# Kernel optimization log

Measured on AMD Instinct MI355X. Metric: run time of the kernel, lower is better.

## Reference

```python
import jax, jax.numpy as jnp
import numpy as np

N_NODES = 100000
N_EDGES = 1600000
D_IN = 128
D_OUT = 128
EPS = 1e-12  # F.normalize default eps


def setup_inputs() -> dict:
    key = jax.random.key(0)
    k1, k2, k3, k4, k5 = jax.random.split(key, 5)
    x = jax.random.normal(k1, (N_NODES, D_IN), dtype=jnp.float32)
    edge_index = jax.random.randint(k2, (2, N_EDGES), 0, N_NODES, dtype=jnp.int64)
    # PyG SAGEConv params: lin_l (neighbor path, with bias), lin_r (root path, no bias)
    s = 1.0 / np.sqrt(D_IN)
    W_l = jax.random.uniform(k3, (D_IN, D_OUT), jnp.float32, -s, s)
    b_l = jax.random.uniform(k4, (D_OUT,), jnp.float32, -s, s)
    W_r = jax.random.uniform(k5, (D_IN, D_OUT), jnp.float32, -s, s)
    return {"x": x, "edge_index": edge_index, "W_l": W_l, "b_l": b_l, "W_r": W_r}


def reference(x, edge_index, W_l, b_l, W_r):
    n = x.shape[0]
    src = edge_index[0]  # message source nodes (x_j)
    dst = edge_index[1]  # aggregation targets (i)
    # gather + mean scatter-reduce
    msg = x[src]                                            # [E, D_IN]
    summed = jax.ops.segment_sum(msg, dst, num_segments=n)  # [N, D_IN]
    cnt = jax.ops.segment_sum(jnp.ones((msg.shape[0],), x.dtype), dst, num_segments=n)
    mean = summed / jnp.maximum(cnt, 1.0)[:, None]
    # lin_l(mean) + lin_r(x), then row-wise L2 normalize
    out = mean @ W_l + b_l + x @ W_r                        # [N, D_OUT]
    norm = jnp.sqrt(jnp.sum(out * out, axis=-1, keepdims=True))
    return out / jnp.maximum(norm, EPS)
```

## Files before the change

### kernel.cpp

```cpp
#include <hip/hip_runtime.h>
#include <hip/hip_bf16.h>

#define N_NODES 100000
#define N_EDGES 1600000
#define D 128
#define TILES (N_NODES / 16)
#define WPB 8
#define NB2 782
#define NPB2 128
#define CAP 4096
#define EPB 8192
#define PBLK 196
#define CVTB 6250
#define PREPB 128

typedef __attribute__((ext_vector_type(4))) float f32x4;
typedef __attribute__((ext_vector_type(8))) short short8;
typedef __attribute__((ext_vector_type(4))) unsigned int u32x4;
typedef __attribute__((ext_vector_type(2))) unsigned int u32x2;

static __device__ __forceinline__ unsigned short f2bf(float f) {
  unsigned u = __float_as_uint(f);
  u += 0x7fffu + ((u >> 16) & 1u);
  return (unsigned short)(u >> 16);
}

static __device__ __forceinline__ void acc4(u32x2 u, float& a0, float& a1,
                                            float& a2, float& a3) {
  a0 += __uint_as_float(u[0] << 16);
  a1 += __uint_as_float(u[0] & 0xffff0000u);
  a2 += __uint_as_float(u[1] << 16);
  a3 += __uint_as_float(u[1] & 0xffff0000u);
}

__global__ __launch_bounds__(256) void fuseA_k(
    const float* __restrict__ x, unsigned* __restrict__ xh,
    const int* __restrict__ ei, int* __restrict__ btail,
    unsigned* __restrict__ part, const float* __restrict__ Wl,
    const float* __restrict__ Wr, unsigned short* __restrict__ wt_g) {
  __shared__ int bh[NB2], lbase[NB2], lcur[NB2];
  int t = threadIdx.x;
  if (blockIdx.x < CVTB) {
    size_t i = (size_t)blockIdx.x * 256 + t;
    const f32x4* p = (const f32x4*)(x + i * 8);
    f32x4 v0 = p[0], v1 = p[1];
    u32x4 o;
    o[0] = ((unsigned)f2bf(v0[1]) << 16) | f2bf(v0[0]);
    o[1] = ((unsigned)f2bf(v0[3]) << 16) | f2bf(v0[2]);
    o[2] = ((unsigned)f2bf(v1[1]) << 16) | f2bf(v1[0]);
    o[3] = ((unsigned)f2bf(v1[3]) << 16) | f2bf(v1[2]);
    *(u32x4*)(xh + i * 4) = o;
    return;
  }
  if (blockIdx.x >= CVTB + PBLK) {
    int i = (blockIdx.x - CVTB - PBLK) * 256 + t;
    int k = i >> 7, c = i & 127;
    float w = (k < 128) ? Wl[k * 128 + c] : Wr[(k - 128) * 128 + c];
    int phys = (k >> 3) ^ (c & 7);
    wt_g[c * 256 + (phys << 3) + (k & 7)] = f2bf(w);
    return;
  }
  for (int i = t; i < NB2; i += 256) { bh[i] = 0; lcur[i] = 0; }
  __syncthreads();
  int base = (blockIdx.x - CVTB) * EPB;
  int end = min(base + EPB, N_EDGES);
  for (int i = base + t; i < end; i += 256)
    atomicAdd(&bh[ei[N_EDGES + i] >> 7], 1);
  __syncthreads();
  for (int i = t; i < NB2; i += 256)
    if (bh[i]) lbase[i] = atomicAdd(&btail[i], bh[i]);
  __syncthreads();
  for (int i = base + t; i < end; i += 256) {
    int dst = ei[N_EDGES + i];
    int src = ei[i];
    int b = dst >> 7;
    int pos = lbase[b] + atomicAdd(&lcur[b], 1);
    if (pos < CAP)
      part[(size_t)b * CAP + pos] =
          ((unsigned)(dst & (NPB2 - 1)) << 17) | (unsigned)src;
  }
}

__global__ __launch_bounds__(512) void p4c_k(unsigned* __restrict__ part,
                                             const int* __restrict__ btail,
                                             int2* __restrict__ pd) {
  __shared__ unsigned s_codes[CAP];
  __shared__ int s_deg[NPB2], s_scan[NPB2], s_off[NPB2];
  int t = threadIdx.x, b = blockIdx.x;
  int ne = min(btail[b], CAP);
  unsigned* pp = part + (size_t)b * CAP;
  for (int i = t; i < ne; i += 512) s_codes[i] = pp[i];
  if (t < NPB2) s_deg[t] = 0;
  __syncthreads();
  for (int i = t; i < ne; i += 512) atomicAdd(&s_deg[s_codes[i] >> 17], 1);
  __syncthreads();
  if (t < NPB2) s_scan[t] = s_deg[t];
  __syncthreads();
  for (int o = 1; o < NPB2; o <<= 1) {
    int u = (t >= o && t < NPB2) ? s_scan[t - o] : 0;
    __syncthreads();
    if (t < NPB2) s_scan[t] += u;
    __syncthreads();
  }
  if (t < NPB2) {
    int deg = s_deg[t];
    int ex = s_scan[t] - deg;
    s_off[t] = ex;
    int node = b * NPB2 + t;
    if (node < N_NODES) {
      int2 v;
      v.x = b * CAP + ex;
      v.y = deg;
      pd[node] = v;
    }
  }
  __syncthreads();
  for (int i = t; i < ne; i += 512) {
    unsigned c = s_codes[i];
    int pos = atomicAdd(&s_off[c >> 17], 1);
    pp[pos] = c & 0x1FFFFu;
  }
}

__global__ __launch_bounds__(256) void gather2_k(const unsigned* __restrict__ xh,
                                                 const unsigned* __restrict__ csr,
                                                 const int2* __restrict__ pd,
                                                 unsigned* __restrict__ mh) {
  int wid = (blockIdx.x * 256 + threadIdx.x) >> 6;
  int lane = threadIdx.x & 63;
  int half = lane >> 5, lh = lane & 31;
  int node = wid * 2 + half;
  if (node >= N_NODES) return;
  int2 v = pd[node];
  int base = v.x;
  int deg = v.y;
  float a0 = 0.f, a1 = 0.f, a2 = 0.f, a3 = 0.f;
  float b0 = 0.f, b1 = 0.f, b2 = 0.f, b3 = 0.f;
  for (int c = 0; c < deg; c += 32) {
    int rem = deg - c;
    int n = min(32, rem);
    int eidx = (lh < rem) ? (int)csr[base + c + lh] : 0;
    int j = 0;
    for (; j + 7 < n; j += 8) {
      int s0 = __shfl(eidx, j, 32);
      int s1 = __shfl(eidx, j + 1, 32);
      int s2 = __shfl(eidx, j + 2, 32);
      int s3 = __shfl(eidx, j + 3, 32);
      int s4 = __shfl(eidx, j + 4, 32);
      int s5 = __shfl(eidx, j + 5, 32);
      int s6 = __shfl(eidx, j + 6, 32);
      int s7 = __shfl(eidx, j + 7, 32);
      u32x2 u0 = *(const u32x2*)(xh + (size_t)s0 * 64 + lh * 2);
      u32x2 u1 = *(const u32x2*)(xh + (size_t)s1 * 64 + lh * 2);
      u32x2 u2 = *(const u32x2*)(xh + (size_t)s2 * 64 + lh * 2);
      u32x2 u3 = *(const u32x2*)(xh + (size_t)s3 * 64 + lh * 2);
      u32x2 u4 = *(const u32x2*)(xh + (size_t)s4 * 64 + lh * 2);
      u32x2 u5 = *(const u32x2*)(xh + (size_t)s5 * 64 + lh * 2);
      u32x2 u6 = *(const u32x2*)(xh + (size_t)s6 * 64 + lh * 2);
      u32x2 u7 = *(const u32x2*)(xh + (size_t)s7 * 64 + lh * 2);
      acc4(u0, a0, a1, a2, a3);
      acc4(u1, b0, b1, b2, b3);
      acc4(u2, a0, a1, a2, a3);
      acc4(u3, b0, b1, b2, b3);
      acc4(u4, a0, a1, a2, a3);
      acc4(u5, b0, b1, b2, b3);
      acc4(u6, a0, a1, a2, a3);
      acc4(u7, b0, b1, b2, b3);
    }
    for (; j + 3 < n; j += 4) {
      int s0 = __shfl(eidx, j, 32);
      int s1 = __shfl(eidx, j + 1, 32);
      int s2 = __shfl(eidx, j + 2, 32);
      int s3 = __shfl(eidx, j + 3, 32);
      u32x2 u0 = *(const u32x2*)(xh + (size_t)s0 * 64 + lh * 2);
      u32x2 u1 = *(const u32x2*)(xh + (size_t)s1 * 64 + lh * 2);
      u32x2 u2 = *(const u32x2*)(xh + (size_t)s2 * 64 + lh * 2);
      u32x2 u3 = *(const u32x2*)(xh + (size_t)s3 * 64 + lh * 2);
      acc4(u0, a0, a1, a2, a3);
      acc4(u1, b0, b1, b2, b3);
      acc4(u2, a0, a1, a2, a3);
      acc4(u3, b0, b1, b2, b3);
    }
    for (; j < n; j++) {
      int s0 = __shfl(eidx, j, 32);
      u32x2 u0 = *(const u32x2*)(xh + (size_t)s0 * 64 + lh * 2);
      acc4(u0, a0, a1, a2, a3);
    }
  }
  float inv = 1.0f / fmaxf((float)deg, 1.0f);
  a0 = (a0 + b0) * inv;
  a1 = (a1 + b1) * inv;
  a2 = (a2 + b2) * inv;
  a3 = (a3 + b3) * inv;
  u32x2 o;
  o[0] = ((unsigned)f2bf(a1) << 16) | f2bf(a0);
  o[1] = ((unsigned)f2bf(a3) << 16) | f2bf(a2);
  *(u32x2*)(mh + (size_t)node * 64 + lh * 2) = o;
}

__global__ __launch_bounds__(512) void fused_k(
    const unsigned* __restrict__ xh, const unsigned* __restrict__ mh,
    const unsigned* __restrict__ wt_g, const float* __restrict__ bl,
    float* __restrict__ out) {
  __shared__ unsigned Wt[16384];

  int tid = threadIdx.x;
  {
    const u32x4* src = (const u32x4*)wt_g;
    u32x4* dst = (u32x4*)Wt;
    #pragma unroll
    for (int it = 0; it < 8; it++) dst[it * 512 + tid] = src[it * 512 + tid];
  }
  __syncthreads();

  int tile = blockIdx.x * WPB + (tid >> 6);
  if (tile >= TILES) return;
  int lane = tid & 63;
  int c0 = lane & 15;
  int g = lane >> 4;
  int row0 = tile * 16;
  const unsigned short* Wt16 = (const unsigned short*)Wt;

  f32x4 acc[8];
  #pragma unroll
  for (int ct = 0; ct < 8; ct++)
    for (int j = 0; j < 4; j++) acc[ct][j] = 0.0f;

  #pragma unroll
  for (int kf = 0; kf < 8; kf++) {
    int koff = (kf & 3) * 32 + g * 8;
    const unsigned short* a_src = (const unsigned short*)((kf < 4) ? mh : xh);
    short8 af = *(const short8*)(a_src + (size_t)(row0 + c0) * D + koff);
    #pragma unroll
    for (int ct = 0; ct < 8; ct++) {
      int c = ct * 16 + c0;
      short8 bf = *(const short8*)&Wt16[c * 256 + ((((kf << 2) + g) ^ (c & 7)) << 3)];
      acc[ct] = __builtin_amdgcn_mfma_f32_16x16x32_bf16(af, bf, acc[ct], 0, 0, 0);
    }
  }

  float ss[4] = {0.f, 0.f, 0.f, 0.f};
  #pragma unroll
  for (int ct = 0; ct < 8; ct++) {
    float bias = bl[ct * 16 + c0];
    #pragma unroll
    for (int j = 0; j < 4; j++) {
      float v = acc[ct][j] + bias;
      acc[ct][j] = v;
      ss[j] += v * v;
    }
  }
  #pragma unroll
  for (int j = 0; j < 4; j++) {
    float s = ss[j];
    s += __shfl_xor(s, 1);
    s += __shfl_xor(s, 2);
    s += __shfl_xor(s, 4);
    s += __shfl_xor(s, 8);
    ss[j] = 1.0f / fmaxf(sqrtf(s), 1e-12f);
  }
  #pragma unroll
  for (int ct = 0; ct < 8; ct++) {
    #pragma unroll
    for (int j = 0; j < 4; j++) {
      out[(size_t)(row0 + g * 4 + j) * D + ct * 16 + c0] = acc[ct][j] * ss[j];
    }
  }
}

extern "C" void kernel_launch(void* const* d_in, const int* in_sizes, int n_in,
                              void* d_out, int out_size, void* d_ws, size_t ws_size,
                              hipStream_t stream) {
  const float* x  = (const float*)d_in[0];
  const int*   ei = (const int*)d_in[1];
  const float* Wl = (const float*)d_in[2];
  const float* bl = (const float*)d_in[3];
  const float* Wr = (const float*)d_in[4];
  float* out = (float*)d_out;

  int* w = (int*)d_ws;
  int* btail = w;
  int2* pd = (int2*)(w + 800);
  unsigned* part = (unsigned*)(w + 200800);
  unsigned short* wt_g = (unsigned short*)(w + 3403872);
  const size_t XH_OFF = 3420256ULL * 4;
  const size_t MH_OFF = XH_OFF + (size_t)N_NODES * D * 2;
  unsigned* xh = (unsigned*)((char*)d_ws + XH_OFF);
  unsigned* mh = (unsigned*)((char*)d_ws + MH_OFF);

  hipMemsetAsync(btail, 0, 800 * sizeof(int), stream);
  fuseA_k<<<CVTB + PBLK + PREPB, 256, 0, stream>>>(x, xh, ei, btail, part,
                                                   Wl, Wr, wt_g);
  p4c_k<<<NB2, 512, 0, stream>>>(part, btail, pd);
  gather2_k<<<12500, 256, 0, stream>>>(xh, part, pd, mh);
  fused_k<<<(TILES + WPB - 1) / WPB, 512, 0, stream>>>(xh, mh, (const unsigned*)wt_g, bl, out);
}
```

Baseline: 152.6 us.

## Replace atomic bucket reservation with per-block histogram and scan partitioning

Splits the fused convert and partition kernel into a conversion kernel plus a three-pass histogram, column scan and scatter. The global atomic reservation on per-bucket tails and its memset go away, and each block's offsets become deterministic, so edges land in source order within each bucket. In exchange it adds three extra kernel launches, reads the edge indices twice, and the partitioning no longer overlaps with the x conversion blocks.

```diff
diff --git a/kernel.cpp b/kernel.cpp
--- a/kernel.cpp
+++ b/kernel.cpp
@@ -33,12 +33,11 @@
   a3 += __uint_as_float(u[1] & 0xffff0000u);
 }
 
-__global__ __launch_bounds__(256) void fuseA_k(
-    const float* __restrict__ x, unsigned* __restrict__ xh,
-    const int* __restrict__ ei, int* __restrict__ btail,
-    unsigned* __restrict__ part, const float* __restrict__ Wl,
-    const float* __restrict__ Wr, unsigned short* __restrict__ wt_g) {
-  __shared__ int bh[NB2], lbase[NB2], lcur[NB2];
+__global__ __launch_bounds__(256) void cvtw_k(const float* __restrict__ x,
+                                              unsigned* __restrict__ xh,
+                                              const float* __restrict__ Wl,
+                                              const float* __restrict__ Wr,
+                                              unsigned short* __restrict__ wt_g) {
   int t = threadIdx.x;
   if (blockIdx.x < CVTB) {
     size_t i = (size_t)blockIdx.x * 256 + t;
@@ -52,42 +51,74 @@
     *(u32x4*)(xh + i * 4) = o;
     return;
   }
-  if (blockIdx.x >= CVTB + PBLK) {
-    int i = (blockIdx.x - CVTB - PBLK) * 256 + t;
-    int k = i >> 7, c = i & 127;
-    float w = (k < 128) ? Wl[k * 128 + c] : Wr[(k - 128) * 128 + c];
-    int phys = (k >> 3) ^ (c & 7);
-    wt_g[c * 256 + (phys << 3) + (k & 7)] = f2bf(w);
-    return;
-  }
-  for (int i = t; i < NB2; i += 256) { bh[i] = 0; lcur[i] = 0; }
-  __syncthreads();
-  int base = (blockIdx.x - CVTB) * EPB;
+  int i = (blockIdx.x - CVTB) * 256 + t;
+  int k = i >> 7, c = i & 127;
+  float w = (k < 128) ? Wl[k * 128 + c] : Wr[(k - 128) * 128 + c];
+  int phys = (k >> 3) ^ (c & 7);
+  wt_g[c * 256 + (phys << 3) + (k & 7)] = f2bf(w);
+}
+
+__global__ __launch_bounds__(256) void p1h_k(const int* __restrict__ ei,
+                                             int* __restrict__ hist) {
+  __shared__ int bh[NB2];
+  int t = threadIdx.x;
+  for (int i = t; i < NB2; i += 256) bh[i] = 0;
+  __syncthreads();
+  int base = blockIdx.x * EPB;
   int end = min(base + EPB, N_EDGES);
   for (int i = base + t; i < end; i += 256)
     atomicAdd(&bh[ei[N_EDGES + i] >> 7], 1);
   __syncthreads();
-  for (int i = t; i < NB2; i += 256)
-    if (bh[i]) lbase[i] = atomicAdd(&btail[i], bh[i]);
-  __syncthreads();
+  for (int i = t; i < NB2; i += 256) hist[blockIdx.x * NB2 + i] = bh[i];
+}
+
+__global__ __launch_bounds__(256) void scanb_k(int* __restrict__ hist,
+                                               int* __restrict__ bcnt) {
+  __shared__ int s[256];
+  int b = blockIdx.x, t = threadIdx.x;
+  int v = (t < PBLK) ? hist[t * NB2 + b] : 0;
+  s[t] = v;
+  __syncthreads();
+  for (int o = 1; o < 256; o <<= 1) {
+    int u = (t >= o) ? s[t - o] : 0;
+    __syncthreads();
+    s[t] += u;
+    __syncthreads();
+  }
+  if (t < PBLK) hist[t * NB2 + b] = s[t] - v;
+  if (t == 0) bcnt[b] = min(s[255], CAP);
+}
+
+__global__ __launch_bounds__(256) void p3c_k(const int* __restrict__ ei,
+                                             const int* __restrict__ hist,
+                                             unsigned* __restrict__ part) {
+  __shared__ int lbase[NB2], lcur[NB2];
+  int t = threadIdx.x, blk = blockIdx.x;
+  for (int i = t; i < NB2; i += 256) {
+    lbase[i] = hist[blk * NB2 + i];
+    lcur[i] = 0;
+  }
+  __syncthreads();
+  int base = blk * EPB;
+  int end = min(base + EPB, N_EDGES);
   for (int i = base + t; i < end; i += 256) {
     int dst = ei[N_EDGES + i];
     int src = ei[i];
     int b = dst >> 7;
-    int pos = lbase[b] + atomicAdd(&lcur[b], 1);
-    if (pos < CAP)
-      part[(size_t)b * CAP + pos] =
+    int rel = lbase[b] + atomicAdd(&lcur[b], 1);
+    if (rel < CAP)
+      part[(size_t)b * CAP + rel] =
           ((unsigned)(dst & (NPB2 - 1)) << 17) | (unsigned)src;
   }
 }
 
 __global__ __launch_bounds__(512) void p4c_k(unsigned* __restrict__ part,
-                                             const int* __restrict__ btail,
+                                             const int* __restrict__ bcnt,
                                              int2* __restrict__ pd) {
   __shared__ unsigned s_codes[CAP];
   __shared__ int s_deg[NPB2], s_scan[NPB2], s_off[NPB2];
   int t = threadIdx.x, b = blockIdx.x;
-  int ne = min(btail[b], CAP);
+  int ne = min(bcnt[b], CAP);
   unsigned* pp = part + (size_t)b * CAP;
   for (int i = t; i < ne; i += 512) s_codes[i] = pp[i];
   if (t < NPB2) s_deg[t] = 0;
@@ -279,19 +310,21 @@
   float* out = (float*)d_out;
 
   int* w = (int*)d_ws;
-  int* btail = w;
-  int2* pd = (int2*)(w + 800);
-  unsigned* part = (unsigned*)(w + 200800);
-  unsigned short* wt_g = (unsigned short*)(w + 3403872);
-  const size_t XH_OFF = 3420256ULL * 4;
+  int* hist = w;
+  int* bcnt = w + 153600;
+  int2* pd = (int2*)(w + 154400);
+  unsigned* part = (unsigned*)(w + 354400);
+  unsigned short* wt_g = (unsigned short*)(w + 3557472);
+  const size_t XH_OFF = 3573856ULL * 4;
   const size_t MH_OFF = XH_OFF + (size_t)N_NODES * D * 2;
   unsigned* xh = (unsigned*)((char*)d_ws + XH_OFF);
   unsigned* mh = (unsigned*)((char*)d_ws + MH_OFF);
 
-  hipMemsetAsync(btail, 0, 800 * sizeof(int), stream);
-  fuseA_k<<<CVTB + PBLK + PREPB, 256, 0, stream>>>(x, xh, ei, btail, part,
-                                                   Wl, Wr, wt_g);
-  p4c_k<<<NB2, 512, 0, stream>>>(part, btail, pd);
+  cvtw_k<<<CVTB + PREPB, 256, 0, stream>>>(x, xh, Wl, Wr, wt_g);
+  p1h_k<<<PBLK, 256, 0, stream>>>(ei, hist);
+  scanb_k<<<NB2, 256, 0, stream>>>(hist, bcnt);
+  p3c_k<<<PBLK, 256, 0, stream>>>(ei, hist, part);
+  p4c_k<<<NB2, 512, 0, stream>>>(part, bcnt, pd);
   gather2_k<<<12500, 256, 0, stream>>>(xh, part, pd, mh);
   fused_k<<<(TILES + WPB - 1) / WPB, 512, 0, stream>>>(xh, mh, (const unsigned*)wt_g, bl, out);
 }
```

After: 142.5 us, median of 2. 6.6% less time.
